# Kernel tuning notes

Hardware: AMD Instinct MI355X
Metric: run time of the kernel (lower is better)

## Reference

```python
import jax, jax.numpy as jnp
import numpy as np

# Model dims (match init_kwargs)
N, IN_CH, EMB_CH, CONV_CH, NUM_HEAD, ORIG_DIM, DEG = 256, 64, 64, 128, 2, 64, 16
C2 = CONV_CH // 2          # GAT hidden dim
NEG_SLOPE = 0.2            # PyG GATv2 default leaky_relu slope
E_TOTAL = N * DEG + N      # random edges + self loops (add_self_loops=True default)


def setup_inputs() -> dict:
    key = jax.random.key(0)
    ks = jax.random.split(key, 32)

    def p(k, shape):
        # xavier-ish: scale by 1/sqrt(fan_in)
        return jax.random.normal(k, shape, jnp.float32) / np.float32(np.sqrt(shape[0]))

    x = jax.random.normal(ks[0], (N, IN_CH), jnp.float32)
    E_emb = jax.random.normal(ks[1], (N, EMB_CH), jnp.float32)
    # random graph + self loops (PyG GATv2Conv adds self loops by default)
    src = jax.random.randint(ks[2], (N * DEG,), 0, N, jnp.int32)
    dst = jax.random.randint(ks[3], (N * DEG,), 0, N, jnp.int32)
    loops = jnp.arange(N, dtype=jnp.int32)
    edge_index = jnp.stack([jnp.concatenate([src, loops]),
                            jnp.concatenate([dst, loops])])  # [2, E_TOTAL]

    inp = {
        "x": x,
        "E_emb": E_emb,
        "edge_index": edge_index,
        "node_proj": p(ks[4], (IN_CH, CONV_CH)),
        "emb_proj": p(ks[5], (EMB_CH, CONV_CH)),
        # Conv1d(conv_ch, conv_ch, k=2, s=2) on a length-2 signal == two matmuls
        "conv_w0": p(ks[6], (CONV_CH, CONV_CH)),   # applied to E channel (stack pos 0)
        "conv_w1": p(ks[7], (CONV_CH, CONV_CH)),   # applied to masked x (stack pos 1)
        "conv_b": jnp.zeros((CONV_CH,), jnp.float32),
        "lin2_w": p(ks[8], (CONV_CH, C2)),
        "lin2_b": jnp.zeros((C2,), jnp.float32),
        "masked_proj": p(ks[9], (C2, C2)),
        "normal_proj": p(ks[10], (C2, C2)),
        # GATv2 layer 1
        "g1_wl": p(ks[11], (C2, NUM_HEAD * C2)), "g1_bl": jnp.zeros((NUM_HEAD * C2,), jnp.float32),
        "g1_wr": p(ks[12], (C2, NUM_HEAD * C2)), "g1_br": jnp.zeros((NUM_HEAD * C2,), jnp.float32),
        "g1_att": p(ks[13], (NUM_HEAD, C2)), "g1_bias": jnp.zeros((C2,), jnp.float32),
        # GATv2 layer 2
        "g2_wl": p(ks[14], (C2, NUM_HEAD * C2)), "g2_bl": jnp.zeros((NUM_HEAD * C2,), jnp.float32),
        "g2_wr": p(ks[15], (C2, NUM_HEAD * C2)), "g2_br": jnp.zeros((NUM_HEAD * C2,), jnp.float32),
        "g2_att": p(ks[16], (NUM_HEAD, C2)), "g2_bias": jnp.zeros((C2,), jnp.float32),
        "rec_w": p(ks[17], (C2, ORIG_DIM)),
        "rec_b": jnp.zeros((ORIG_DIM,), jnp.float32),
    }
    return inp


def _forward(x, E_emb, edge_index,
             node_proj, emb_proj, conv_w0, conv_w1, conv_b, lin2_w, lin2_b,
             masked_proj, normal_proj,
             g1_wl, g1_bl, g1_wr, g1_br, g1_att, g1_bias,
             g2_wl, g2_bl, g2_wr, g2_br, g2_att, g2_bias,
             rec_w, rec_b):
    n = x.shape[0]
    src, dst = edge_index[0], edge_index[1]

    x_p = x @ node_proj          # [N, CONV_CH]
    E_p = E_emb @ emb_proj       # [N, CONV_CH]
    # conv1d(k=2,s=2) over stacked [E_p, masked_x] -> base is the unmasked result
    x_w1 = x_p @ conv_w1                          # per-row contribution of x
    base = E_p @ conv_w0 + x_w1 + conv_b          # [N, CONV_CH]

    def gatv2(h, wl, bl, wr, br, att, bias):
        # PyG GATv2Conv, concat=False (head mean), negative_slope=0.2, eval mode
        xl = (h @ wl + bl).reshape(n, NUM_HEAD, C2)   # source transform
        xr = (h @ wr + br).reshape(n, NUM_HEAD, C2)   # target transform
        e = jax.nn.leaky_relu(xl[src] + xr[dst], NEG_SLOPE)   # [E, H, C2]
        logit = jnp.einsum('ehc,hc->eh', e, att)              # [E, H]
        mx = jax.ops.segment_max(logit, dst, num_segments=n)  # per-target max
        w = jnp.exp(logit - mx[dst])
        denom = jax.ops.segment_sum(w, dst, num_segments=n)
        alpha = w / (denom[dst] + 1e-16)
        out = jax.ops.segment_sum(xl[src] * alpha[:, :, None], dst, num_segments=n)
        return out.mean(axis=1) + bias                        # [N, C2]

    def per_node(i):
        # masking row i of x_p zeroes its contribution to the conv output
        h = jnp.tanh(base.at[i].add(-x_w1[i]))
        m = h @ lin2_w + lin2_b                               # [N, C2]
        proj = m @ normal_proj
        proj = proj.at[i].set(m[i] @ masked_proj)
        g = jax.nn.elu(gatv2(proj, g1_wl, g1_bl, g1_wr, g1_br, g1_att, g1_bias))
        g = jax.nn.elu(gatv2(g, g2_wl, g2_bl, g2_wr, g2_br, g2_att, g2_bias))
        return g[i] @ rec_w + rec_b                           # only row i is used

    recon = jax.vmap(per_node)(jnp.arange(n))                 # [N, ORIG_DIM]
    return jnp.tanh(recon)


def reference(x, E_emb, edge_index,
              node_proj, emb_proj, conv_w0, conv_w1, conv_b, lin2_w, lin2_b,
              masked_proj, normal_proj,
              g1_wl, g1_bl, g1_wr, g1_br, g1_att, g1_bias,
              g2_wl, g2_bl, g2_wr, g2_br, g2_att, g2_bias,
              rec_w, rec_b):
    return _forward(x, E_emb, edge_index,
                    node_proj, emb_proj, conv_w0, conv_w1, conv_b, lin2_w, lin2_b,
                    masked_proj, normal_proj,
                    g1_wl, g1_bl, g1_wr, g1_br, g1_att, g1_bias,
                    g2_wl, g2_bl, g2_wr, g2_br, g2_att, g2_bias,
                    rec_w, rec_b)
```

## Files before the change

### kernel.cpp

```cpp
#include <hip/hip_runtime.h>
#include <hip/hip_bf16.h>


#define NN 256
#define EDGE_CAP 96
#define E2_CAP 64
#define E_CAP 6144
#define M_CAP 8

#define OFF_G1ATT  115136
#define OFF_G1BIAS 115264
#define OFF_G2WL   115328
#define OFF_G2BL   123520
#define OFF_G2WR   123648
#define OFF_G2BR   131840
#define OFF_G2ATT  131968
#define OFF_G2BIAS 132096
#define OFF_RECW   132160
#define OFF_RECB   136256
#define W_TOTAL    136320

__device__ float g_w[W_TOTAL];
__device__ __align__(16) float g_xl0[NN*128];
__device__ __align__(16) float g_xr0[NN*128];
__device__ __align__(16) float g_xlV[NN*128];
__device__ __align__(16) float g_xrV[NN*128];
__device__ __align__(16) float g_xl2_0[NN*128];
__device__ __align__(16) float g_num[NN*128];
__device__ float g_m[NN*2], g_den[NN*2];
__device__ float g_elog[E_CAP*2];
__device__ int   g_in_ptr[NN+1], g_out_ptr[NN+1];
__device__ int   g_in_src[E_CAP], g_out_dst[E_CAP];
__device__ int   g_f32;

typedef const void* cvp;
typedef unsigned short ushort8v __attribute__((ext_vector_type(8)));

__device__ __forceinline__ float b2f(__hip_bfloat16 v) { return __bfloat162float(v); }
__device__ __forceinline__ float bfbits(unsigned short u) {
  union { unsigned int i; float f; } c; c.i = ((unsigned int)u) << 16; return c.f;
}

template<typename T> __device__ __forceinline__ float ldv(cvp p, int i);
template<> __device__ __forceinline__ float ldv<float>(cvp p, int i) {
  return ((const float*)p)[i];
}
template<> __device__ __forceinline__ float ldv<__hip_bfloat16>(cvp p, int i) {
  return b2f(((const __hip_bfloat16*)p)[i]);
}

template<typename T>
__device__ __forceinline__ void stage8k(float* dst, cvp src, int elemOff, int t)
{
  if constexpr (sizeof(T) == 4) {
    const float4* s = (const float4*)((const float*)src + elemOff);
    float4* d = (float4*)dst;
    #pragma unroll
    for (int r = 0; r < 8; ++r) d[r*256 + t] = s[r*256 + t];
  } else {
    const ushort8v* s = (const ushort8v*)((const __hip_bfloat16*)src + elemOff);
    #pragma unroll
    for (int r = 0; r < 4; ++r) {
      const ushort8v v = s[r*256 + t];
      float4* d = (float4*)(dst + (r*256 + t)*8);
      float4 lo, hi;
      lo.x = bfbits(v[0]); lo.y = bfbits(v[1]); lo.z = bfbits(v[2]); lo.w = bfbits(v[3]);
      hi.x = bfbits(v[4]); hi.y = bfbits(v[5]); hi.z = bfbits(v[6]); hi.w = bfbits(v[7]);
      d[0] = lo; d[1] = hi;
    }
  }
}

template<typename T>
__device__ __forceinline__ void stage4k(float* dst, cvp src, int t)
{
  if constexpr (sizeof(T) == 4) {
    const float4* s = (const float4*)src;
    float4* d = (float4*)dst;
    #pragma unroll
    for (int r = 0; r < 4; ++r) d[r*256 + t] = s[r*256 + t];
  } else {
    const ushort8v* s = (const ushort8v*)src;
    #pragma unroll
    for (int r = 0; r < 2; ++r) {
      const ushort8v v = s[r*256 + t];
      float4* d = (float4*)(dst + (r*256 + t)*8);
      float4 lo, hi;
      lo.x = bfbits(v[0]); lo.y = bfbits(v[1]); lo.z = bfbits(v[2]); lo.w = bfbits(v[3]);
      hi.x = bfbits(v[4]); hi.y = bfbits(v[5]); hi.z = bfbits(v[6]); hi.w = bfbits(v[7]);
      d[0] = lo; d[1] = hi;
    }
  }
}

struct __align__(16) DenseS {
  float WB[8192];
  float sx[64], sE[64];
  float sxp[128], sEp[128];
  float sA[128];
  float scb[128], sl2b[64], sbl[128], sbr[128];
  float sh0[128], shm[128];
  float sm0[64], sMm[64], sp0[64], sV[64];
  float pp[4][128], qq[4][128];
  float pk[4][64], qk[4][64];
};

template<typename T>
__device__ void dense_body(DenseS& S, int j, int t,
    cvp x, cvp E_emb, cvp np, cvp ep, cvp cw0, cvp cw1, cvp cbp,
    cvp l2w, cvp l2bp, cvp mp, cvp npj, cvp wl, cvp blp, cvp wr, cvp brp)
{
  const int c1 = t & 127, kh = t >> 7;
  const int c6 = t & 63,  kg = t >> 6;

  stage8k<T>(S.WB, np, 0, t);
  if (t < 64)        S.sx[t]    = ldv<T>(x,     j*64 + t);
  else if (t < 128)  S.sE[t-64] = ldv<T>(E_emb, j*64 + (t-64));
  __syncthreads();
  { float a = 0.f;
    #pragma unroll
    for (int kk = 0; kk < 32; ++kk) { const int k = kh*32+kk; a += S.sx[k]*S.WB[k*128+c1]; }
    S.pp[kh][c1] = a; }
  __syncthreads();

  stage8k<T>(S.WB, ep, 0, t);
  if (t < 128) S.sxp[t] = S.pp[0][t] + S.pp[1][t];
  __syncthreads();
  { float a = 0.f;
    #pragma unroll
    for (int kk = 0; kk < 32; ++kk) { const int k = kh*32+kk; a += S.sE[k]*S.WB[k*128+c1]; }
    S.qq[kh][c1] = a; }
  __syncthreads();

  stage8k<T>(S.WB, cw1, 0, t);
  if (t < 128) S.sEp[t] = S.qq[0][t] + S.qq[1][t];
  __syncthreads();
  { float a = 0.f;
    #pragma unroll
    for (int kk = 0; kk < 32; ++kk) { const int k = kh*32+kk; a += S.sxp[k]*S.WB[k*128+c1]; }
    S.pp[kh][c1] = a; }
  __syncthreads();

  stage8k<T>(S.WB, cw1, 8192, t);
  __syncthreads();
  { float a = 0.f;
    #pragma unroll
    for (int kk = 0; kk < 32; ++kk) { const int k = kh*32+kk; a += S.sxp[64+k]*S.WB[k*128+c1]; }
    S.pp[2+kh][c1] = a; }
  __syncthreads();

  stage8k<T>(S.WB, cw0, 0, t);
  if (t < 128) S.sA[t] = S.pp[0][t]+S.pp[1][t]+S.pp[2][t]+S.pp[3][t];
  __syncthreads();
  { float a = 0.f;
    #pragma unroll
    for (int kk = 0; kk < 32; ++kk) { const int k = kh*32+kk; a += S.sEp[k]*S.WB[k*128+c1]; }
    S.qq[kh][c1] = a; }
  __syncthreads();

  stage8k<T>(S.WB, cw0, 8192, t);
  if (t < 128) S.scb[t] = ldv<T>(cbp, t);
  __syncthreads();
  { float a = 0.f;
    #pragma unroll
    for (int kk = 0; kk < 32; ++kk) { const int k = kh*32+kk; a += S.sEp[64+k]*S.WB[k*128+c1]; }
    S.qq[2+kh][c1] = a; }
  __syncthreads();

  stage8k<T>(S.WB, l2w, 0, t);
  if (t < 128) {
    const float ew0 = S.qq[0][t]+S.qq[1][t]+S.qq[2][t]+S.qq[3][t];
    S.sh0[t] = tanhf(ew0 + S.sA[t] + S.scb[t]);
    S.shm[t] = tanhf(ew0 + S.scb[t]);
  } else if (t < 192) S.sl2b[t-128] = ldv<T>(l2bp, t-128);
  __syncthreads();
  { float a = 0.f, b = 0.f;
    #pragma unroll
    for (int kk = 0; kk < 32; ++kk) {
      const int k = kg*32+kk; const float w = S.WB[k*64+c6];
      a += S.sh0[k]*w; b += S.shm[k]*w;
    }
    S.pk[kg][c6] = a; S.qk[kg][c6] = b; }
  __syncthreads();

  stage4k<T>(S.WB,        npj, t);
  stage4k<T>(S.WB + 4096, mp,  t);
  if (t < 64) {
    S.sm0[t] = S.sl2b[t] + S.pk[0][t]+S.pk[1][t]+S.pk[2][t]+S.pk[3][t];
    S.sMm[t] = S.sl2b[t] + S.qk[0][t]+S.qk[1][t]+S.qk[2][t]+S.qk[3][t];
  }
  __syncthreads();
  { float a = 0.f, b = 0.f;
    #pragma unroll
    for (int kk = 0; kk < 16; ++kk) {
      const int k = kg*16+kk;
      a += S.sm0[k]*S.WB[k*64+c6];
      b += S.sMm[k]*S.WB[4096 + k*64+c6];
    }
    S.pk[kg][c6] = a; S.qk[kg][c6] = b; }
  __syncthreads();

  stage8k<T>(S.WB, wl, 0, t);
  if (t < 64)       S.sp0[t]    = S.pk[0][t]+S.pk[1][t]+S.pk[2][t]+S.pk[3][t];
  else if (t < 128) S.sV[t-64]  = S.qk[0][t-64]+S.qk[1][t-64]+S.qk[2][t-64]+S.qk[3][t-64];
  else              S.sbl[t-128] = ldv<T>(blp, t-128);
  __syncthreads();
  { float l = 0.f, lv = 0.f;
    #pragma unroll
    for (int kk = 0; kk < 32; ++kk) {
      const int k = kh*32+kk; const float w = S.WB[k*128+c1];
      l += S.sp0[k]*w; lv += S.sV[k]*w;
    }
    S.pp[kh][c1] = l; S.qq[kh][c1] = lv; }
  __syncthreads();

  stage8k<T>(S.WB, wr, 0, t);
  if (t < 128) {
    g_xl0[j*128+t] = S.sbl[t] + S.pp[0][t] + S.pp[1][t];
    g_xlV[j*128+t] = S.sbl[t] + S.qq[0][t] + S.qq[1][t];
  } else S.sbr[t-128] = ldv<T>(brp, t-128);
  __syncthreads();
  { float r = 0.f, rv = 0.f;
    #pragma unroll
    for (int kk = 0; kk < 32; ++kk) {
      const int k = kh*32+kk; const float w = S.WB[k*128+c1];
      r += S.sp0[k]*w; rv += S.sV[k]*w;
    }
    S.pp[kh][c1] = r; S.qq[kh][c1] = rv; }
  __syncthreads();
  if (t < 128) {
    g_xr0[j*128+t] = S.sbr[t] + S.pp[0][t] + S.pp[1][t];
    g_xrV[j*128+t] = S.sbr[t] + S.qq[0][t] + S.qq[1][t];
  }
}

__global__ __launch_bounds__(256) void k_fused(
    cvp x, cvp E_emb, cvp node_proj, cvp emb_proj,
    cvp conv_w0, cvp conv_w1, cvp conv_b, cvp lin2_w, cvp lin2_b,
    cvp masked_proj, cvp normal_proj,
    cvp g1_wl, cvp g1_bl, cvp g1_wr, cvp g1_br, cvp g1_att, cvp g1_bias,
    cvp g2_wl, cvp g2_bl, cvp g2_wr, cvp g2_br, cvp g2_att, cvp g2_bias,
    cvp rec_w, cvp rec_b,
    int n, const int* __restrict__ ei, int E)
{
  const int t = threadIdx.x, b = blockIdx.x;
  __shared__ int s_cnt;
  __shared__ DenseS DS;
  if (t == 0) s_cnt = 0;
  __syncthreads();
  {
    const __hip_bfloat16* xb = (const __hip_bfloat16*)x;
    const int lim = n < 4096 ? n : 4096;
    int c = 0;
    for (int i = t; i < lim; i += 256) {
      const float v = b2f(xb[i]);
      if (!(fabsf(v) <= 16.f)) c++;
    }
    if (c) atomicAdd(&s_cnt, c);
  }
  __syncthreads();
  const int f = (s_cnt > 64) ? 1 : 0;

  if (b < NN) {
    if (f) dense_body<float>(DS, b, t, x, E_emb, node_proj, emb_proj,
                             conv_w0, conv_w1, conv_b, lin2_w, lin2_b,
                             masked_proj, normal_proj, g1_wl, g1_bl, g1_wr, g1_br);
    else   dense_body<__hip_bfloat16>(DS, b, t, x, E_emb, node_proj, emb_proj,
                             conv_w0, conv_w1, conv_b, lin2_w, lin2_b,
                             masked_proj, normal_proj, g1_wl, g1_bl, g1_wr, g1_br);
    return;
  }

  if (t == 0) g_f32 = f;
  {
    cvp segs2[10] = {g1_att, g1_bias, g2_wl, g2_bl, g2_wr, g2_br,
                     g2_att, g2_bias, rec_w, rec_b};
    const int o2[11] = {OFF_G1ATT, OFF_G1BIAS, OFF_G2WL, OFF_G2BL, OFF_G2WR,
                        OFF_G2BR, OFF_G2ATT, OFF_G2BIAS, OFF_RECW, OFF_RECB,
                        W_TOTAL};
    if (f) {
      for (int s = 0; s < 10; ++s) {
        const float* pf = (const float*)segs2[s];
        const int off = o2[s], len = o2[s+1] - off;
        for (int i2 = t; i2 < len; i2 += 256) g_w[off+i2] = pf[i2];
      }
    } else {
      for (int s = 0; s < 10; ++s) {
        const __hip_bfloat16* pb = (const __hip_bfloat16*)segs2[s];
        const int off = o2[s], len = o2[s+1] - off;
        for (int i2 = t; i2 < len; i2 += 256) g_w[off+i2] = b2f(pb[i2]);
      }
    }
  }
  __shared__ int cin[NN], cou[NN], pin[NN], pou[NN];
  if (E > E_CAP) E = E_CAP;
  cin[t] = 0; cou[t] = 0;
  __syncthreads();
  for (int e = t; e < E; e += 256) {
    atomicAdd(&cin[ei[E+e] & (NN-1)], 1);
    atomicAdd(&cou[ei[e]   & (NN-1)], 1);
  }
  __syncthreads();
  pin[t] = cin[t]; pou[t] = cou[t];
  __syncthreads();
  for (int off = 1; off < NN; off <<= 1) {
    int a = 0, c = 0;
    if (t >= off) { a = pin[t-off]; c = pou[t-off]; }
    __syncthreads();
    if (t >= off) { pin[t] += a; pou[t] += c; }
    __syncthreads();
  }
  const int exi = pin[t] - cin[t];
  const int exo = pou[t] - cou[t];
  g_in_ptr[t] = exi; g_out_ptr[t] = exo;
  if (t == NN-1) { g_in_ptr[NN] = pin[t]; g_out_ptr[NN] = pou[t]; }
  cin[t] = exi; cou[t] = exo;
  __syncthreads();
  for (int e = t; e < E; e += 256) {
    const int s = ei[e] & (NN-1), d = ei[E+e] & (NN-1);
    g_in_src[atomicAdd(&cin[d], 1)] = s;
    g_out_dst[atomicAdd(&cou[s], 1)] = d;
  }
}

__global__ __launch_bounds__(256) void k_l1base()
{
  const int j = blockIdx.x, t = threadIdx.x;
  __shared__ __align__(16) float sxr[128];
  __shared__ __align__(16) float satt[128];
  __shared__ float slog[2][EDGE_CAP], sw[2][EDGE_CAP];
  __shared__ float sinv[2], sg1[64], spA[4][64], spB[4][64], sx2[2][128];
  __shared__ int ssrc[EDGE_CAP];
  const int base = g_in_ptr[j];
  int nE = g_in_ptr[j+1] - base;
  if (nE > EDGE_CAP) nE = EDGE_CAP;
  if (t < 128) { sxr[t] = g_xr0[j*128+t]; satt[t] = g_w[OFF_G1ATT + t]; }
  for (int e = t; e < nE; e += 256) ssrc[e] = g_in_src[base+e];
  __syncthreads();
  for (int idx = t; idx < nE*2; idx += 256) {
    const int e = idx >> 1, h = idx & 1, s = ssrc[e];
    const float4* x4 = (const float4*)(g_xl0 + s*128 + h*64);
    const float4* r4 = (const float4*)(sxr + h*64);
    const float4* a4 = (const float4*)(satt + h*64);
    float acc = 0.f;
    #pragma unroll
    for (int q = 0; q < 16; ++q) {
      const float4 xv = x4[q], rv = r4[q], av = a4[q];
      float v0 = xv.x + rv.x; v0 = v0 > 0.f ? v0 : 0.2f*v0;
      float v1 = xv.y + rv.y; v1 = v1 > 0.f ? v1 : 0.2f*v1;
      float v2 = xv.z + rv.z; v2 = v2 > 0.f ? v2 : 0.2f*v2;
      float v3 = xv.w + rv.w; v3 = v3 > 0.f ? v3 : 0.2f*v3;
      acc += av.x*v0 + av.y*v1 + av.z*v2 + av.w*v3;
    }
    slog[h][e] = acc;
    g_elog[(base+e)*2+h] = acc;
  }
  __syncthreads();
  if (t < 128) {
    const int h = t >> 6, lane = t & 63;
    float m = -1e30f;
    for (int e = lane; e < nE; e += 64) m = fmaxf(m, slog[h][e]);
    for (int o = 1; o < 64; o <<= 1) m = fmaxf(m, __shfl_xor(m, o));
    float ssum = 0.f;
    for (int e = lane; e < nE; e += 64) {
      const float w = __expf(slog[h][e]-m); sw[h][e] = w; ssum += w;
    }
    for (int o = 1; o < 64; o <<= 1) ssum += __shfl_xor(ssum, o);
    if (lane == 0) {
      sinv[h] = 1.f/(ssum + 1e-16f);
      g_m[j*2+h] = m; g_den[j*2+h] = ssum;
    }
  }
  __syncthreads();
  {
    const int grp = t >> 6, c = t & 63;
    float a0 = 0.f, a1 = 0.f;
    for (int e = grp; e < nE; e += 4) {
      const float* xs = g_xl0 + ssrc[e]*128;
      a0 += sw[0][e]*xs[c];
      a1 += sw[1][e]*xs[64+c];
    }
    spA[grp][c] = a0; spB[grp][c] = a1;
  }
  __syncthreads();
  if (t < 64) {
    const float a0 = spA[0][t]+spA[1][t]+spA[2][t]+spA[3][t];
    const float a1 = spB[0][t]+spB[1][t]+spB[2][t]+spB[3][t];
    g_num[j*128+t] = a0; g_num[j*128+64+t] = a1;
    float g = 0.5f*(a0*sinv[0] + a1*sinv[1]) + g_w[OFF_G1BIAS + t];
    g = g > 0.f ? g : expm1f(g);
    sg1[t] = g;
  }
  __syncthreads();
  {
    const int c = t & 127, half = t >> 7;
    float acc = 0.f;
    const int k0 = half*32;
    #pragma unroll
    for (int kk = 0; kk < 32; ++kk) {
      const int k = k0 + kk;
      acc += sg1[k]*g_w[OFF_G2WL + k*128+c];
    }
    sx2[half][c] = acc;
  }
  __syncthreads();
  if (t < 128) g_xl2_0[j*128+t] = g_w[OFF_G2BL + t] + sx2[0][t] + sx2[1][t];
}

struct __align__(16) P3s {
  float xl2e[E2_CAP*128];
  float rtmp[M_CAP*128];
  float g1m[M_CAP*64];
  float sgi[64];
  float sxlVi[128], sxl0i[128], sxri[128];
  float satt[128], satt2[128];
  float xr2i[128], sg[64];
  float spE[2][2][64];
  float slog[2][E2_CAP], sw[2][E2_CAP];
  float sinv[2];
  int   slotOf[NN];
  unsigned char isInN[NN];
  int   ssrc2[E2_CAP], listM[M_CAP], listCh[E2_CAP];
  int   nM, nCh;
};

__device__ __forceinline__ void delta_one(P3s& S, int m, int nMl, int i, int t)
{
  if (m >= nMl) return;
  const int lt = t - 128, h = lt >> 6, c = lt & 63;
  const int j = S.listM[m];
  const float mj = g_m[j*2+h];
  float u = S.sxlVi[lt] + g_xr0[j*128+lt];
  u = u > 0.f ? u : 0.2f*u;
  float ln = S.satt[lt]*u;
  for (int o = 1; o < 64; o <<= 1) ln += __shfl_xor(ln, o);
  const float wn1 = __expf(ln - mj);
  const int jb = g_in_ptr[j], jd = g_in_ptr[j+1] - jb;
  float wo = 0.f; int cnt = 0;
  for (int p = c; p < jd; p += 64)
    if (g_in_src[jb+p] == i) { wo += __expf(g_elog[(jb+p)*2+h] - mj); cnt++; }
  for (int o = 1; o < 64; o <<= 1) {
    wo += __shfl_xor(wo, o); cnt += __shfl_xor(cnt, o);
  }
  const float dd = (float)cnt*wn1 - wo;
  const float dn = (float)cnt*wn1*S.sxlVi[lt] - wo*S.sxl0i[lt];
  S.rtmp[m*128+lt] = (g_num[j*128+lt] + dn) / (g_den[j*2+h] + dd + 1e-16f);
}

__global__ __launch_bounds__(256) void k_periter(void* out)
{
  const int i = blockIdx.x, t = threadIdx.x;
  __shared__ P3s S;

  if (t < NN) { S.slotOf[t] = -1; S.isInN[t] = 0; }
  if (t == 0) S.nM = 0;
  if (t < 128) {
    S.satt[t]  = g_w[OFF_G1ATT + t];
    S.satt2[t] = g_w[OFF_G2ATT + t];
    S.sxlVi[t] = g_xlV[i*128+t];
    S.sxl0i[t] = g_xl0[i*128+t];
    S.sxri[t]  = g_xrV[i*128+t];
  }
  __syncthreads();
  if (t == 0) S.slotOf[i] = 0;

  const int b2 = g_in_ptr[i];
  int nE2 = g_in_ptr[i+1] - b2;
  if (nE2 > E2_CAP) nE2 = E2_CAP;
  for (int e = t; e < nE2; e += 256) {
    const int s = g_in_src[b2+e];
    S.ssrc2[e] = s;
    S.isInN[s] = 1;
  }
  __syncthreads();

  const int ob = g_out_ptr[i], onE = g_out_ptr[i+1] - ob;
  for (int e = t; e < onE; e += 256) {
    const int d = g_out_dst[ob+e];
    if (d != i && S.isInN[d]) {
      if (atomicCAS(&S.slotOf[d], -1, -2) == -1) {
        const int p = atomicAdd(&S.nM, 1);
        if (p < M_CAP) { S.listM[p] = d; S.slotOf[d] = p + 1; }
        else S.slotOf[d] = -1;
      }
    }
  }
  for (int idx = t; idx < nE2*2; idx += 256) {
    const int e = idx >> 1, h = idx & 1, s = S.ssrc2[e];
    const float* xls = (s == i) ? (S.sxlVi + h*64) : (g_xl0 + s*128 + h*64);
    const float4* x4 = (const float4*)xls;
    const float4* r4 = (const float4*)(S.sxri + h*64);
    const float4* a4 = (const float4*)(S.satt + h*64);
    float acc = 0.f;
    #pragma unroll
    for (int q = 0; q < 16; ++q) {
      const float4 xv = x4[q], rv = r4[q], av = a4[q];
      float v0 = xv.x + rv.x; v0 = v0 > 0.f ? v0 : 0.2f*v0;
      float v1 = xv.y + rv.y; v1 = v1 > 0.f ? v1 : 0.2f*v1;
      float v2 = xv.z + rv.z; v2 = v2 > 0.f ? v2 : 0.2f*v2;
      float v3 = xv.w + rv.w; v3 = v3 > 0.f ? v3 : 0.2f*v3;
      acc += av.x*v0 + av.y*v1 + av.z*v2 + av.w*v3;
    }
    S.slog[h][e] = acc;
  }
  __syncthreads();
  const int nMl = S.nM > M_CAP ? M_CAP : S.nM;

  if (t < 128) {
    const int h = t >> 6, lane = t & 63;
    float m = -1e30f;
    for (int e = lane; e < nE2; e += 64) m = fmaxf(m, S.slog[h][e]);
    for (int o = 1; o < 64; o <<= 1) m = fmaxf(m, __shfl_xor(m, o));
    float ssum = 0.f;
    for (int e = lane; e < nE2; e += 64) {
      const float w = __expf(S.slog[h][e]-m); S.sw[h][e] = w; ssum += w;
    }
    for (int o = 1; o < 64; o <<= 1) ssum += __shfl_xor(ssum, o);
    if (lane == 0) S.sinv[h] = 1.f/(ssum + 1e-16f);
  } else {
    delta_one(S, 0, nMl, i, t);
  }
  __syncthreads();

  if (t < 128) {
    const int g2 = t >> 6, c = t & 63;
    float a0 = 0.f, a1 = 0.f;
    for (int e = g2; e < nE2; e += 2) {
      const int s = S.ssrc2[e];
      const float* xs = (s == i) ? S.sxlVi : (g_xl0 + s*128);
      a0 += S.sw[0][e]*xs[c];
      a1 += S.sw[1][e]*xs[64+c];
    }
    S.spE[g2][0][c] = a0; S.spE[g2][1][c] = a1;
  } else {
    delta_one(S, 1, nMl, i, t);
  }
  __syncthreads();

  if (t < 64) {
    const float a0 = S.spE[0][0][t] + S.spE[1][0][t];
    const float a1 = S.spE[0][1][t] + S.spE[1][1][t];
    float g = 0.5f*(a0*S.sinv[0] + a1*S.sinv[1]) + g_w[OFF_G1BIAS + t];
    g = g > 0.f ? g : expm1f(g);
    S.sgi[t] = g;
  } else if (t == 64) {
    int nc = 0;
    for (int e = 0; e < nE2; ++e)
      if (S.slotOf[S.ssrc2[e]] >= 0) S.listCh[nc++] = e;
    S.nCh = nc;
  } else if (t >= 128) {
    delta_one(S, 2, nMl, i, t);
  }
  __syncthreads();

  for (int m = 3; m < nMl; ++m) {
    if (t >= 128) delta_one(S, m, nMl, i, t);
    __syncthreads();
  }

  if (t < 128) {
    float v = g_w[OFF_G2BR + t];
    #pragma unroll
    for (int k = 0; k < 64; ++k) v += S.sgi[k]*g_w[OFF_G2WR + k*128+t];
    S.xr2i[t] = v;
  } else {
    for (int idx = t - 128; idx < nMl*64; idx += 128) {
      const int m = idx >> 6, c = idx & 63;
      float g = 0.5f*(S.rtmp[m*128+c] + S.rtmp[m*128+64+c]) + g_w[OFF_G1BIAS + c];
      g = g > 0.f ? g : expm1f(g);
      S.g1m[m*64+c] = g;
    }
  }
  __syncthreads();

  for (int idx = t; idx < nE2*32; idx += 256) {
    const int e = idx >> 5, q = idx & 31;
    ((float4*)S.xl2e)[e*32 + q] =
        *((const float4*)(g_xl2_0 + S.ssrc2[e]*128) + q);
  }
  __syncthreads();
  for (int idx = t; idx < S.nCh*128; idx += 256) {
    const int e = S.listCh[idx >> 7], c = idx & 127;
    const int sl = S.slotOf[S.ssrc2[e]];
    const float* g1r = (sl == 0) ? S.sgi : (S.g1m + (sl-1)*64);
    float v = g_w[OFF_G2BL + c];
    #pragma unroll
    for (int k = 0; k < 64; ++k) v += g1r[k]*g_w[OFF_G2WL + k*128+c];
    S.xl2e[e*128+c] = v;
  }
  __syncthreads();

  for (int idx = t; idx < nE2*2; idx += 256) {
    const int e = idx >> 1, h = idx & 1;
    const float4* x4 = (const float4*)(S.xl2e + e*128 + h*64);
    const float4* r4 = (const float4*)(S.xr2i + h*64);
    const float4* a4 = (const float4*)(S.satt2 + h*64);
    float acc = 0.f;
    #pragma unroll
    for (int q = 0; q < 16; ++q) {
      const float4 xv = x4[q], rv = r4[q], av = a4[q];
      float v0 = xv.x + rv.x; v0 = v0 > 0.f ? v0 : 0.2f*v0;
      float v1 = xv.y + rv.y; v1 = v1 > 0.f ? v1 : 0.2f*v1;
      float v2 = xv.z + rv.z; v2 = v2 > 0.f ? v2 : 0.2f*v2;
      float v3 = xv.w + rv.w; v3 = v3 > 0.f ? v3 : 0.2f*v3;
      acc += av.x*v0 + av.y*v1 + av.z*v2 + av.w*v3;
    }
    S.slog[h][e] = acc;
  }
  __syncthreads();

  if (t < 128) {
    const int h = t >> 6, lane = t & 63;
    float m = -1e30f;
    for (int e = lane; e < nE2; e += 64) m = fmaxf(m, S.slog[h][e]);
    for (int o = 1; o < 64; o <<= 1) m = fmaxf(m, __shfl_xor(m, o));
    float ssum = 0.f;
    for (int e = lane; e < nE2; e += 64) {
      const float w = __expf(S.slog[h][e]-m); S.sw[h][e] = w; ssum += w;
    }
    for (int o = 1; o < 64; o <<= 1) ssum += __shfl_xor(ssum, o);
    if (lane == 0) S.sinv[h] = 1.f/(ssum + 1e-16f);
  }
  __syncthreads();

  if (t < 128) {
    const int g2 = t >> 6, c = t & 63;
    float a0 = 0.f, a1 = 0.f;
    for (int e = g2; e < nE2; e += 2) {
      a0 += S.sw[0][e]*S.xl2e[e*128 + c];
      a1 += S.sw[1][e]*S.xl2e[e*128 + 64 + c];
    }
    S.spE[g2][0][c] = a0; S.spE[g2][1][c] = a1;
  }
  __syncthreads();
  if (t < 64) {
    const float a0 = S.spE[0][0][t] + S.spE[1][0][t];
    const float a1 = S.spE[0][1][t] + S.spE[1][1][t];
    float g = 0.5f*(a0*S.sinv[0] + a1*S.sinv[1]) + g_w[OFF_G2BIAS + t];
    g = g > 0.f ? g : expm1f(g);
    S.sg[t] = g;
  }
  __syncthreads();

  if (t < 64) {
    float v = g_w[OFF_RECB + t];
    #pragma unroll
    for (int c = 0; c < 64; ++c) v += S.sg[c]*g_w[OFF_RECW + c*64+t];
    const float r = tanhf(v);
    if (g_f32) ((float*)out)[i*64+t] = r;
    else       ((__hip_bfloat16*)out)[i*64+t] = __float2bfloat16(r);
  }
}

extern "C" void kernel_launch(void* const* d_in, const int* in_sizes, int n_in,
                              void* d_out, int out_size, void* d_ws, size_t ws_size,
                              hipStream_t stream)
{
  const int* ei = (const int*)d_in[2];
  const int E = in_sizes[2] / 2;

  k_fused<<<NN+1, 256, 0, stream>>>(
      d_in[0], d_in[1], d_in[3], d_in[4], d_in[5], d_in[6], d_in[7],
      d_in[8], d_in[9], d_in[10], d_in[11], d_in[12], d_in[13], d_in[14],
      d_in[15], d_in[16], d_in[17], d_in[18], d_in[19], d_in[20], d_in[21],
      d_in[22], d_in[23], d_in[24], d_in[25],
      in_sizes[0], ei, E);
  k_l1base<<<NN, 256, 0, stream>>>();
  k_periter<<<NN, 256, 0, stream>>>(d_out);
}
```

Measured before the change: 170.8 us.

## Recompute two-hop GAT layer-1 neighborhood per node instead of delta-correcting base

```diff
diff --git a/kernel.cpp b/kernel.cpp
--- a/kernel.cpp
+++ b/kernel.cpp
@@ -3,10 +3,9 @@
 
 
 #define NN 256
-#define EDGE_CAP 96
 #define E2_CAP 64
+#define D_CAP 64
 #define E_CAP 6144
-#define M_CAP 8
 
 #define OFF_G1ATT  115136
 #define OFF_G1BIAS 115264
@@ -25,10 +24,6 @@
 __device__ __align__(16) float g_xr0[NN*128];
 __device__ __align__(16) float g_xlV[NN*128];
 __device__ __align__(16) float g_xrV[NN*128];
-__device__ __align__(16) float g_xl2_0[NN*128];
-__device__ __align__(16) float g_num[NN*128];
-__device__ float g_m[NN*2], g_den[NN*2];
-__device__ float g_elog[E_CAP*2];
 __device__ int   g_in_ptr[NN+1], g_out_ptr[NN+1];
 __device__ int   g_in_src[E_CAP], g_out_dst[E_CAP];
 __device__ int   g_f32;
@@ -323,25 +318,61 @@
   }
 }
 
-__global__ __launch_bounds__(256) void k_l1base()
+struct __align__(16) P3s {
+  float xl2e[E2_CAP*128];
+  float slogS[E2_CAP][D_CAP][2];
+  float g1p[E2_CAP][64];
+  int   susrc[E2_CAP][D_CAP];
+  float sxlVi[128], sxri[128];
+  float satt[128], satt2[128];
+  float xr2i[128];
+  float sgi[64], sg[64];
+  float slog[2][E2_CAP], sw[2][E2_CAP];
+  float spE[4][2][64];
+  float sinv[2];
+  int   ssrc2[E2_CAP], sS_base[E2_CAP], sS_deg[E2_CAP], soff[E2_CAP+1];
+  int   Ltot;
+};
+
+__global__ __launch_bounds__(256) void k_periter(void* out)
 {
-  const int j = blockIdx.x, t = threadIdx.x;
-  __shared__ __align__(16) float sxr[128];
-  __shared__ __align__(16) float satt[128];
-  __shared__ float slog[2][EDGE_CAP], sw[2][EDGE_CAP];
-  __shared__ float sinv[2], sg1[64], spA[4][64], spB[4][64], sx2[2][128];
-  __shared__ int ssrc[EDGE_CAP];
-  const int base = g_in_ptr[j];
-  int nE = g_in_ptr[j+1] - base;
-  if (nE > EDGE_CAP) nE = EDGE_CAP;
-  if (t < 128) { sxr[t] = g_xr0[j*128+t]; satt[t] = g_w[OFF_G1ATT + t]; }
-  for (int e = t; e < nE; e += 256) ssrc[e] = g_in_src[base+e];
-  __syncthreads();
-  for (int idx = t; idx < nE*2; idx += 256) {
-    const int e = idx >> 1, h = idx & 1, s = ssrc[e];
-    const float4* x4 = (const float4*)(g_xl0 + s*128 + h*64);
-    const float4* r4 = (const float4*)(sxr + h*64);
-    const float4* a4 = (const float4*)(satt + h*64);
+  const int i = blockIdx.x, t = threadIdx.x;
+  const int warp = t >> 6, lane = t & 63;
+  __shared__ P3s S;
+
+  if (t < 128) {
+    S.satt[t]  = g_w[OFF_G1ATT + t];
+    S.satt2[t] = g_w[OFF_G2ATT + t];
+    S.sxlVi[t] = g_xlV[i*128+t];
+    S.sxri[t]  = g_xrV[i*128+t];
+  }
+
+  const int b2 = g_in_ptr[i];
+  int nE2 = g_in_ptr[i+1] - b2;
+  if (nE2 > E2_CAP) nE2 = E2_CAP;
+  for (int e = t; e < nE2; e += 256) {
+    const int s = g_in_src[b2+e];
+    S.ssrc2[e] = s;
+    const int sb = g_in_ptr[s];
+    int sd = g_in_ptr[s+1] - sb;
+    if (sd > D_CAP) sd = D_CAP;
+    if (s == i) sd = 0;
+    S.sS_base[e] = sb; S.sS_deg[e] = sd;
+  }
+  __syncthreads();
+  if (t == 0) {
+    int acc = 0;
+    for (int e = 0; e < nE2; ++e) { S.soff[e] = acc; acc += S.sS_deg[e]; }
+    S.soff[nE2] = acc; S.Ltot = acc;
+  }
+  __syncthreads();
+
+  for (int idx = t; idx < nE2*2; idx += 256) {
+    const int e = idx >> 1, h = idx & 1, s = S.ssrc2[e];
+    const float* xls = (s == i) ? (S.sxlVi + h*64) : (g_xl0 + s*128 + h*64);
+    const float4* x4 = (const float4*)xls;
+    const float4* r4 = (const float4*)(S.sxri + h*64);
+    const float4* a4 = (const float4*)(S.satt + h*64);
     float acc = 0.f;
     #pragma unroll
     for (int q = 0; q < 16; ++q) {
@@ -352,144 +383,21 @@
       float v3 = xv.w + rv.w; v3 = v3 > 0.f ? v3 : 0.2f*v3;
       acc += av.x*v0 + av.y*v1 + av.z*v2 + av.w*v3;
     }
-    slog[h][e] = acc;
-    g_elog[(base+e)*2+h] = acc;
-  }
-  __syncthreads();
-  if (t < 128) {
-    const int h = t >> 6, lane = t & 63;
-    float m = -1e30f;
-    for (int e = lane; e < nE; e += 64) m = fmaxf(m, slog[h][e]);
-    for (int o = 1; o < 64; o <<= 1) m = fmaxf(m, __shfl_xor(m, o));
-    float ssum = 0.f;
-    for (int e = lane; e < nE; e += 64) {
-      const float w = __expf(slog[h][e]-m); sw[h][e] = w; ssum += w;
-    }
-    for (int o = 1; o < 64; o <<= 1) ssum += __shfl_xor(ssum, o);
-    if (lane == 0) {
-      sinv[h] = 1.f/(ssum + 1e-16f);
-      g_m[j*2+h] = m; g_den[j*2+h] = ssum;
-    }
-  }
-  __syncthreads();
-  {
-    const int grp = t >> 6, c = t & 63;
-    float a0 = 0.f, a1 = 0.f;
-    for (int e = grp; e < nE; e += 4) {
-      const float* xs = g_xl0 + ssrc[e]*128;
-      a0 += sw[0][e]*xs[c];
-      a1 += sw[1][e]*xs[64+c];
-    }
-    spA[grp][c] = a0; spB[grp][c] = a1;
-  }
-  __syncthreads();
-  if (t < 64) {
-    const float a0 = spA[0][t]+spA[1][t]+spA[2][t]+spA[3][t];
-    const float a1 = spB[0][t]+spB[1][t]+spB[2][t]+spB[3][t];
-    g_num[j*128+t] = a0; g_num[j*128+64+t] = a1;
-    float g = 0.5f*(a0*sinv[0] + a1*sinv[1]) + g_w[OFF_G1BIAS + t];
-    g = g > 0.f ? g : expm1f(g);
-    sg1[t] = g;
-  }
-  __syncthreads();
-  {
-    const int c = t & 127, half = t >> 7;
-    float acc = 0.f;
-    const int k0 = half*32;
-    #pragma unroll
-    for (int kk = 0; kk < 32; ++kk) {
-      const int k = k0 + kk;
-      acc += sg1[k]*g_w[OFF_G2WL + k*128+c];
-    }
-    sx2[half][c] = acc;
-  }
-  __syncthreads();
-  if (t < 128) g_xl2_0[j*128+t] = g_w[OFF_G2BL + t] + sx2[0][t] + sx2[1][t];
-}
-
-struct __align__(16) P3s {
-  float xl2e[E2_CAP*128];
-  float rtmp[M_CAP*128];
-  float g1m[M_CAP*64];
-  float sgi[64];
-  float sxlVi[128], sxl0i[128], sxri[128];
-  float satt[128], satt2[128];
-  float xr2i[128], sg[64];
-  float spE[2][2][64];
-  float slog[2][E2_CAP], sw[2][E2_CAP];
-  float sinv[2];
-  int   slotOf[NN];
-  unsigned char isInN[NN];
-  int   ssrc2[E2_CAP], listM[M_CAP], listCh[E2_CAP];
-  int   nM, nCh;
-};
-
-__device__ __forceinline__ void delta_one(P3s& S, int m, int nMl, int i, int t)
-{
-  if (m >= nMl) return;
-  const int lt = t - 128, h = lt >> 6, c = lt & 63;
-  const int j = S.listM[m];
-  const float mj = g_m[j*2+h];
-  float u = S.sxlVi[lt] + g_xr0[j*128+lt];
-  u = u > 0.f ? u : 0.2f*u;
-  float ln = S.satt[lt]*u;
-  for (int o = 1; o < 64; o <<= 1) ln += __shfl_xor(ln, o);
-  const float wn1 = __expf(ln - mj);
-  const int jb = g_in_ptr[j], jd = g_in_ptr[j+1] - jb;
-  float wo = 0.f; int cnt = 0;
-  for (int p = c; p < jd; p += 64)
-    if (g_in_src[jb+p] == i) { wo += __expf(g_elog[(jb+p)*2+h] - mj); cnt++; }
-  for (int o = 1; o < 64; o <<= 1) {
-    wo += __shfl_xor(wo, o); cnt += __shfl_xor(cnt, o);
-  }
-  const float dd = (float)cnt*wn1 - wo;
-  const float dn = (float)cnt*wn1*S.sxlVi[lt] - wo*S.sxl0i[lt];
-  S.rtmp[m*128+lt] = (g_num[j*128+lt] + dn) / (g_den[j*2+h] + dd + 1e-16f);
-}
-
-__global__ __launch_bounds__(256) void k_periter(void* out)
-{
-  const int i = blockIdx.x, t = threadIdx.x;
-  __shared__ P3s S;
-
-  if (t < NN) { S.slotOf[t] = -1; S.isInN[t] = 0; }
-  if (t == 0) S.nM = 0;
-  if (t < 128) {
-    S.satt[t]  = g_w[OFF_G1ATT + t];
-    S.satt2[t] = g_w[OFF_G2ATT + t];
-    S.sxlVi[t] = g_xlV[i*128+t];
-    S.sxl0i[t] = g_xl0[i*128+t];
-    S.sxri[t]  = g_xrV[i*128+t];
-  }
-  __syncthreads();
-  if (t == 0) S.slotOf[i] = 0;
-
-  const int b2 = g_in_ptr[i];
-  int nE2 = g_in_ptr[i+1] - b2;
-  if (nE2 > E2_CAP) nE2 = E2_CAP;
-  for (int e = t; e < nE2; e += 256) {
-    const int s = g_in_src[b2+e];
-    S.ssrc2[e] = s;
-    S.isInN[s] = 1;
-  }
-  __syncthreads();
-
-  const int ob = g_out_ptr[i], onE = g_out_ptr[i+1] - ob;
-  for (int e = t; e < onE; e += 256) {
-    const int d = g_out_dst[ob+e];
-    if (d != i && S.isInN[d]) {
-      if (atomicCAS(&S.slotOf[d], -1, -2) == -1) {
-        const int p = atomicAdd(&S.nM, 1);
-        if (p < M_CAP) { S.listM[p] = d; S.slotOf[d] = p + 1; }
-        else S.slotOf[d] = -1;
-      }
-    }
-  }
-  for (int idx = t; idx < nE2*2; idx += 256) {
-    const int e = idx >> 1, h = idx & 1, s = S.ssrc2[e];
-    const float* xls = (s == i) ? (S.sxlVi + h*64) : (g_xl0 + s*128 + h*64);
-    const float4* x4 = (const float4*)xls;
-    const float4* r4 = (const float4*)(S.sxri + h*64);
+    S.slog[h][e] = acc;
+  }
+  const int L2n = S.Ltot * 2;
+  for (int idx = t; idx < L2n; idx += 256) {
+    const int pair = idx >> 1, h = idx & 1;
+    int lo = 0, hi = nE2 - 1;
+    while (lo < hi) { const int mid = (lo+hi+1) >> 1;
+                      if (S.soff[mid] <= pair) lo = mid; else hi = mid-1; }
+    const int sI = lo, e = pair - S.soff[sI];
+    const int sn = S.ssrc2[sI];
+    const int u = g_in_src[S.sS_base[sI] + e];
+    if (h == 0) S.susrc[sI][e] = u;
+    const float4* x4 = (const float4*)((u == i) ? (S.sxlVi + h*64)
+                                                : (g_xl0 + u*128 + h*64));
+    const float4* r4 = (const float4*)(g_xr0 + sn*128 + h*64);
     const float4* a4 = (const float4*)(S.satt + h*64);
     float acc = 0.f;
     #pragma unroll
@@ -501,88 +409,89 @@
       float v3 = xv.w + rv.w; v3 = v3 > 0.f ? v3 : 0.2f*v3;
       acc += av.x*v0 + av.y*v1 + av.z*v2 + av.w*v3;
     }
-    S.slog[h][e] = acc;
-  }
-  __syncthreads();
-  const int nMl = S.nM > M_CAP ? M_CAP : S.nM;
-
-  if (t < 128) {
-    const int h = t >> 6, lane = t & 63;
+    S.slogS[sI][e][h] = acc;
+  }
+  __syncthreads();
+
+  if (t < 128) {
+    const int h = t >> 6, l = t & 63;
     float m = -1e30f;
-    for (int e = lane; e < nE2; e += 64) m = fmaxf(m, S.slog[h][e]);
+    for (int e = l; e < nE2; e += 64) m = fmaxf(m, S.slog[h][e]);
     for (int o = 1; o < 64; o <<= 1) m = fmaxf(m, __shfl_xor(m, o));
     float ssum = 0.f;
-    for (int e = lane; e < nE2; e += 64) {
+    for (int e = l; e < nE2; e += 64) {
       const float w = __expf(S.slog[h][e]-m); S.sw[h][e] = w; ssum += w;
     }
     for (int o = 1; o < 64; o <<= 1) ssum += __shfl_xor(ssum, o);
-    if (lane == 0) S.sinv[h] = 1.f/(ssum + 1e-16f);
-  } else {
-    delta_one(S, 0, nMl, i, t);
-  }
-  __syncthreads();
-
-  if (t < 128) {
-    const int g2 = t >> 6, c = t & 63;
+    if (l == 0) S.sinv[h] = 1.f/(ssum + 1e-16f);
+  }
+  __syncthreads();
+
+  {
     float a0 = 0.f, a1 = 0.f;
-    for (int e = g2; e < nE2; e += 2) {
+    for (int e = warp; e < nE2; e += 4) {
       const int s = S.ssrc2[e];
       const float* xs = (s == i) ? S.sxlVi : (g_xl0 + s*128);
-      a0 += S.sw[0][e]*xs[c];
-      a1 += S.sw[1][e]*xs[64+c];
-    }
-    S.spE[g2][0][c] = a0; S.spE[g2][1][c] = a1;
-  } else {
-    delta_one(S, 1, nMl, i, t);
+      a0 += S.sw[0][e]*xs[lane];
+      a1 += S.sw[1][e]*xs[64+lane];
+    }
+    S.spE[warp][0][lane] = a0; S.spE[warp][1][lane] = a1;
   }
   __syncthreads();
 
   if (t < 64) {
-    const float a0 = S.spE[0][0][t] + S.spE[1][0][t];
-    const float a1 = S.spE[0][1][t] + S.spE[1][1][t];
+    const float a0 = S.spE[0][0][t]+S.spE[1][0][t]+S.spE[2][0][t]+S.spE[3][0][t];
+    const float a1 = S.spE[0][1][t]+S.spE[1][1][t]+S.spE[2][1][t]+S.spE[3][1][t];
     float g = 0.5f*(a0*S.sinv[0] + a1*S.sinv[1]) + g_w[OFF_G1BIAS + t];
     g = g > 0.f ? g : expm1f(g);
     S.sgi[t] = g;
-  } else if (t == 64) {
-    int nc = 0;
-    for (int e = 0; e < nE2; ++e)
-      if (S.slotOf[S.ssrc2[e]] >= 0) S.listCh[nc++] = e;
-    S.nCh = nc;
-  } else if (t >= 128) {
-    delta_one(S, 2, nMl, i, t);
-  }
-  __syncthreads();
-
-  for (int m = 3; m < nMl; ++m) {
-    if (t >= 128) delta_one(S, m, nMl, i, t);
-    __syncthreads();
-  }
+  }
+  __syncthreads();
+
+  for (int sI = warp; sI < nE2; sI += 4) {
+    const int d = S.sS_deg[sI];
+    if (d == 0) continue;
+    float l0 = (lane < d) ? S.slogS[sI][lane][0] : -1e30f;
+    float l1 = (lane < d) ? S.slogS[sI][lane][1] : -1e30f;
+    for (int o = 1; o < 64; o <<= 1) {
+      l0 = fmaxf(l0, __shfl_xor(l0, o));
+      l1 = fmaxf(l1, __shfl_xor(l1, o));
+    }
+    float w0 = 0.f, w1 = 0.f;
+    if (lane < d) {
+      w0 = __expf(S.slogS[sI][lane][0] - l0);
+      w1 = __expf(S.slogS[sI][lane][1] - l1);
+      S.slogS[sI][lane][0] = w0;
+      S.slogS[sI][lane][1] = w1;
+    }
+    float s0 = w0, s1 = w1;
+    for (int o = 1; o < 64; o <<= 1) { s0 += __shfl_xor(s0, o); s1 += __shfl_xor(s1, o); }
+    const float inv0 = 1.f/(s0 + 1e-16f), inv1 = 1.f/(s1 + 1e-16f);
+    float a0 = 0.f, a1 = 0.f;
+    for (int e = 0; e < d; ++e) {
+      const int u = S.susrc[sI][e];
+      const float* xu = (u == i) ? S.sxlVi : (g_xl0 + u*128);
+      a0 += S.slogS[sI][e][0]*xu[lane];
+      a1 += S.slogS[sI][e][1]*xu[64+lane];
+    }
+    float g = 0.5f*(a0*inv0 + a1*inv1) + g_w[OFF_G1BIAS + lane];
+    g = g > 0.f ? g : expm1f(g);
+    S.g1p[sI][lane] = g;
+  }
+  __syncthreads();
 
   if (t < 128) {
     float v = g_w[OFF_G2BR + t];
     #pragma unroll
     for (int k = 0; k < 64; ++k) v += S.sgi[k]*g_w[OFF_G2WR + k*128+t];
     S.xr2i[t] = v;
-  } else {
-    for (int idx = t - 128; idx < nMl*64; idx += 128) {
-      const int m = idx >> 6, c = idx & 63;
-      float g = 0.5f*(S.rtmp[m*128+c] + S.rtmp[m*128+64+c]) + g_w[OFF_G1BIAS + c];
-      g = g > 0.f ? g : expm1f(g);
-      S.g1m[m*64+c] = g;
-    }
-  }
-  __syncthreads();
-
-  for (int idx = t; idx < nE2*32; idx += 256) {
-    const int e = idx >> 5, q = idx & 31;
-    ((float4*)S.xl2e)[e*32 + q] =
-        *((const float4*)(g_xl2_0 + S.ssrc2[e]*128) + q);
-  }
-  __syncthreads();
-  for (int idx = t; idx < S.nCh*128; idx += 256) {
-    const int e = S.listCh[idx >> 7], c = idx & 127;
-    const int sl = S.slotOf[S.ssrc2[e]];
-    const float* g1r = (sl == 0) ? S.sgi : (S.g1m + (sl-1)*64);
+  }
+  __syncthreads();
+
+  for (int idx = t; idx < nE2*128; idx += 256) {
+    const int e = idx >> 7, c = idx & 127;
+    const int s = S.ssrc2[e];
+    const float* g1r = (s == i) ? S.sgi : S.g1p[e];
     float v = g_w[OFF_G2BL + c];
     #pragma unroll
     for (int k = 0; k < 64; ++k) v += g1r[k]*g_w[OFF_G2WL + k*128+c];
@@ -610,32 +519,31 @@
   __syncthreads();
 
   if (t < 128) {
-    const int h = t >> 6, lane = t & 63;
+    const int h = t >> 6, l = t & 63;
     float m = -1e30f;
-    for (int e = lane; e < nE2; e += 64) m = fmaxf(m, S.slog[h][e]);
+    for (int e = l; e < nE2; e += 64) m = fmaxf(m, S.slog[h][e]);
     for (int o = 1; o < 64; o <<= 1) m = fmaxf(m, __shfl_xor(m, o));
     float ssum = 0.f;
-    for (int e = lane; e < nE2; e += 64) {
+    for (int e = l; e < nE2; e += 64) {
       const float w = __expf(S.slog[h][e]-m); S.sw[h][e] = w; ssum += w;
     }
     for (int o = 1; o < 64; o <<= 1) ssum += __shfl_xor(ssum, o);
-    if (lane == 0) S.sinv[h] = 1.f/(ssum + 1e-16f);
-  }
-  __syncthreads();
-
-  if (t < 128) {
-    const int g2 = t >> 6, c = t & 63;
+    if (l == 0) S.sinv[h] = 1.f/(ssum + 1e-16f);
+  }
+  __syncthreads();
+
+  {
     float a0 = 0.f, a1 = 0.f;
-    for (int e = g2; e < nE2; e += 2) {
-      a0 += S.sw[0][e]*S.xl2e[e*128 + c];
-      a1 += S.sw[1][e]*S.xl2e[e*128 + 64 + c];
-    }
-    S.spE[g2][0][c] = a0; S.spE[g2][1][c] = a1;
+    for (int e = warp; e < nE2; e += 4) {
+      a0 += S.sw[0][e]*S.xl2e[e*128 + lane];
+      a1 += S.sw[1][e]*S.xl2e[e*128 + 64 + lane];
+    }
+    S.spE[warp][0][lane] = a0; S.spE[warp][1][lane] = a1;
   }
   __syncthreads();
   if (t < 64) {
-    const float a0 = S.spE[0][0][t] + S.spE[1][0][t];
-    const float a1 = S.spE[0][1][t] + S.spE[1][1][t];
+    const float a0 = S.spE[0][0][t]+S.spE[1][0][t]+S.spE[2][0][t]+S.spE[3][0][t];
+    const float a1 = S.spE[0][1][t]+S.spE[1][1][t]+S.spE[2][1][t]+S.spE[3][1][t];
     float g = 0.5f*(a0*S.sinv[0] + a1*S.sinv[1]) + g_w[OFF_G2BIAS + t];
     g = g > 0.f ? g : expm1f(g);
     S.sg[t] = g;
@@ -665,6 +573,5 @@
       d_in[15], d_in[16], d_in[17], d_in[18], d_in[19], d_in[20], d_in[21],
       d_in[22], d_in[23], d_in[24], d_in[25],
       in_sizes[0], ei, E);
-  k_l1base<<<NN, 256, 0, stream>>>();
   k_periter<<<NN, 256, 0, stream>>>(d_out);
 }
```

Measured after the change: 186.4 us. 1.09x slower.
